# Performance work log

Hardware: AMD Instinct MI355X
Metric: run time of the kernel (lower is better)

## Reference

```python
import jax, jax.numpy as jnp
import numpy as np

NUM_HEADS = 4

def _proj(x, w, b):
    # Conv1d kernel_size=1 == pointwise linear over channels: [B, Cin, N] -> [B, Cout, N]
    return jnp.einsum('oi,bin->bon', w, x) + b[None, :, None]

def setup_inputs() -> dict:
    key = jax.random.key(0)
    ks = jax.random.split(key, 11)
    B, D, N = 8, 256, 2048
    inp = {
        'query': jax.random.normal(ks[0], (B, D, N), jnp.float32),
        'key':   jax.random.normal(ks[1], (B, D, N), jnp.float32),
        'value': jax.random.normal(ks[2], (B, D, N), jnp.float32),
        'w_q': jax.random.normal(ks[3], (D, D), jnp.float32) * (1.0 / np.sqrt(D)),
        'b_q': jax.random.normal(ks[4], (D,), jnp.float32) * 0.02,
        'w_k': jax.random.normal(ks[5], (D, D), jnp.float32) * (1.0 / np.sqrt(D)),
        'b_k': jax.random.normal(ks[6], (D,), jnp.float32) * 0.02,
        'w_v': jax.random.normal(ks[7], (D, D), jnp.float32) * (1.0 / np.sqrt(D)),
        'b_v': jax.random.normal(ks[8], (D,), jnp.float32) * 0.02,
        'w_m': jax.random.normal(ks[9], (D, D), jnp.float32) * (1.0 / np.sqrt(D)),
        'b_m': jax.random.normal(ks[10], (D,), jnp.float32) * 0.02,
    }
    return inp

def reference(query, key, value, w_q, b_q, w_k, b_k, w_v, b_v, w_m, b_m):
    B, D, N = query.shape
    H = NUM_HEADS
    d = D // H  # head dim (outer slot of channel split, matching torch .view)
    q = _proj(query, w_q, b_q).reshape(B, d, H, N)
    k = _proj(key,   w_k, b_k).reshape(B, d, H, N)
    v = _proj(value, w_v, b_v).reshape(B, d, H, N)
    scale = jnp.asarray(1.0 / np.sqrt(d), q.dtype)
    scores = jnp.einsum('bdhn,bdhm->bhnm', q, k) * scale  # [B,H,N,N]
    prob = jax.nn.softmax(scores, axis=-1)
    x = jnp.einsum('bhnm,bdhm->bdhn', prob, v)            # [B,d,H,N]
    out = _proj(x.reshape(B, D, N), w_m, b_m)             # [B,D,N]
    return out
```

## Files before the change

kernel.cpp:

```cpp
#include <hip/hip_runtime.h>
#include <cstdint>
#include <cstddef>

typedef unsigned short u16;
typedef unsigned int   u32;
typedef __attribute__((ext_vector_type(4))) float f32x4;
typedef __attribute__((ext_vector_type(16))) float f32x16;
typedef __attribute__((ext_vector_type(8))) short bf16x8;
typedef __attribute__((ext_vector_type(4))) unsigned short u16x4;
typedef __attribute__((ext_vector_type(2))) u32 u32x2;
typedef __attribute__((ext_vector_type(4))) u32 u32x4;

#define DEVI static __device__ __forceinline__
#define MFMA16(a,b,c) __builtin_amdgcn_mfma_f32_16x16x32_bf16((a),(b),(c),0,0,0)
#define MFMA32(a,b,c) __builtin_amdgcn_mfma_f32_32x32x16_bf16((a),(b),(c),0,0,0)

DEVI u16 f2b(float f) {
  u32 u = __builtin_bit_cast(u32, f);
  u32 r = u + 0x7fffu + ((u >> 16) & 1u);
  return (u16)(r >> 16);
}

DEVI u32 pkbf(float a, float b) {
  u32 r;
  asm("v_cvt_pk_bf16_f32 %0, %1, %2" : "=v"(r) : "v"(a), "v"(b));
  return r;
}

DEVI void load_lds16(const void* g, void* l) {
  __builtin_amdgcn_global_load_lds(
      (const __attribute__((address_space(1))) u32*)g,
      (__attribute__((address_space(3))) u32*)l, 16, 0, 0);
}

DEVI int perm_o(int o) { return 4 * (o & 63) + (o >> 6); }

__global__ __launch_bounds__(256) void k_prep_w(
    const float* __restrict__ wq, const float* __restrict__ wk,
    const float* __restrict__ wv, const float* __restrict__ wm,
    const float* __restrict__ bq, const float* __restrict__ bk, const float* __restrict__ bv,
    u16* __restrict__ WQ, u16* __restrict__ WK, u16* __restrict__ WV, u16* __restrict__ WM,
    float* __restrict__ BQ, float* __restrict__ BK, float* __restrict__ BV)
{
  int row = blockIdx.x, t = threadIdx.x, m = blockIdx.y;
  if (m == 0)      WQ[row * 256 + t] = f2b(wq[perm_o(row) * 256 + t]);
  else if (m == 1) WK[row * 256 + t] = f2b(wk[perm_o(row) * 256 + t]);
  else if (m == 2) WV[row * 256 + t] = f2b(wv[perm_o(row) * 256 + t]);
  else if (m == 3) WM[row * 256 + t] = f2b(wm[row * 256 + perm_o(t)]);
  else if (row == 0) {
    BQ[t] = bq[perm_o(t)];
    BK[t] = bk[perm_o(t)];
    BV[t] = bv[perm_o(t)];
  }
}

__global__ __launch_bounds__(256) void k_transpose(
    const float* __restrict__ q, const float* __restrict__ k, const float* __restrict__ v,
    u16* __restrict__ xq, u16* __restrict__ xk, u16* __restrict__ xv)
{
  __shared__ u16 tile[64][68];
  const int N = 2048, D = 256;
  int n0 = blockIdx.x * 64, c0 = blockIdx.y * 64;
  int b = blockIdx.z & 7, which = blockIdx.z >> 3;
  const float* src = (which == 0 ? q : which == 1 ? k : v) + (size_t)b * D * N;
  u16* dst = (which == 0 ? xq : which == 1 ? xk : xv) + (size_t)b * N * D;
  int t = threadIdx.x;
  int cl = t >> 4, ng = t & 15;
#pragma unroll
  for (int cc = 0; cc < 4; ++cc) {
    int c = cl + 16 * cc;
    f32x4 val = *(const f32x4*)&src[(size_t)(c0 + c) * N + n0 + ng * 4];
#pragma unroll
    for (int j = 0; j < 4; ++j) tile[c][ng * 4 + j] = f2b(val[j]);
  }
  __syncthreads();
  int n = t & 63, cq = t >> 6;
  union { u16 s[16]; u32x4 v4[2]; } pk;
#pragma unroll
  for (int j = 0; j < 16; ++j) pk.s[j] = tile[cq * 16 + j][n];
  u32x4* o = (u32x4*)&dst[(size_t)(n0 + n) * D + c0 + cq * 16];
  o[0] = pk.v4[0];
  o[1] = pk.v4[1];
}

template<int EPI>
__global__ __launch_bounds__(256, 4) void k_gemm(
    const u16* __restrict__ A, long sA,
    const u16* __restrict__ Bm, long sB,
    const float* __restrict__ bias,
    void* __restrict__ out, long sOut)
{
  __shared__ u16 lA[64 * 64];
  __shared__ u16 lB[64 * 64];
  int t = threadIdx.x, b = blockIdx.z;
  const u16* Ab = A + (size_t)b * sA + (size_t)blockIdx.x * 64 * 256;
  const u16* Bb = Bm + (size_t)b * sB + (size_t)blockIdx.y * 64 * 256;
  int l = t & 63, w = t >> 6, g = l >> 4, col = l & 15;
  int wr = w >> 1, wc = w & 1;
  f32x4 acc[2][2] = {};
  u32 sOf[2], sDs[2];
#pragma unroll
  for (int j = 0; j < 2; ++j) {
    int c = t + 256 * j;
    sOf[j] = (u32)(((c >> 3) * 512) + (((c & 7) ^ ((c >> 3) & 7)) << 4));
    sDs[j] = (u32)(c * 16);
  }
  for (int k0 = 0; k0 < 256; k0 += 64) {
    __syncthreads();
#pragma unroll
    for (int j = 0; j < 2; ++j) {
      load_lds16((const char*)(Ab + k0) + sOf[j], (char*)lA + sDs[j]);
      load_lds16((const char*)(Bb + k0) + sOf[j], (char*)lB + sDs[j]);
    }
    asm volatile("s_waitcnt vmcnt(0)" ::: "memory");
    __syncthreads();
#pragma unroll
    for (int kc = 0; kc < 2; ++kc) {
      bf16x8 af[2], bfr[2];
#pragma unroll
      for (int mt = 0; mt < 2; ++mt) {
        int row = wr * 32 + mt * 16 + col;
        af[mt] = *(const bf16x8*)((const char*)lA + row * 128 + (((kc * 4 + g) ^ (row & 7)) << 4));
      }
#pragma unroll
      for (int nt = 0; nt < 2; ++nt) {
        int row = wc * 32 + nt * 16 + col;
        bfr[nt] = *(const bf16x8*)((const char*)lB + row * 128 + (((kc * 4 + g) ^ (row & 7)) << 4));
      }
#pragma unroll
      for (int mt = 0; mt < 2; ++mt)
#pragma unroll
        for (int nt = 0; nt < 2; ++nt)
          acc[mt][nt] = MFMA16(af[mt], bfr[nt], acc[mt][nt]);
    }
  }
  if (EPI == 0) {
    u16* o = (u16*)out + (size_t)b * sOut;
#pragma unroll
    for (int nt = 0; nt < 2; ++nt) {
      int op = blockIdx.y * 64 + wc * 32 + nt * 16 + col;
      int hh = op >> 6, ii = op & 63;
      float bv = bias[op];
#pragma unroll
      for (int mt = 0; mt < 2; ++mt) {
        int nbase = blockIdx.x * 64 + wr * 32 + mt * 16 + g * 4;
#pragma unroll
        for (int r = 0; r < 4; ++r)
          o[((size_t)(hh * 2048 + nbase + r)) * 64 + ii] = f2b(acc[mt][nt][r] + bv);
      }
    }
  } else if (EPI == 1) {
    u16* o = (u16*)out + (size_t)b * sOut;
#pragma unroll
    for (int mt = 0; mt < 2; ++mt)
#pragma unroll
      for (int r = 0; r < 4; ++r) {
        int row = blockIdx.x * 64 + wr * 32 + mt * 16 + g * 4 + r;
        float bv = bias[row];
#pragma unroll
        for (int nt = 0; nt < 2; ++nt) {
          int cn = blockIdx.y * 64 + wc * 32 + nt * 16 + col;
          o[(size_t)row * 2048 + cn] = f2b(acc[mt][nt][r] + bv);
        }
      }
  } else {
    float* o = (float*)out + (size_t)b * sOut;
#pragma unroll
    for (int mt = 0; mt < 2; ++mt)
#pragma unroll
      for (int r = 0; r < 4; ++r) {
        int row = blockIdx.x * 64 + wr * 32 + mt * 16 + g * 4 + r;
        float bv = bias[row];
#pragma unroll
        for (int nt = 0; nt < 2; ++nt) {
          int cn = blockIdx.y * 64 + wc * 32 + nt * 16 + col;
          o[(size_t)row * 2048 + cn] = acc[mt][nt][r] + bv;
        }
      }
  }
}

__global__ __launch_bounds__(256, 4) void k_attn(
    const u16* __restrict__ Qt, const u16* __restrict__ Kt,
    const u16* __restrict__ Vw, u16* __restrict__ Xws)
{
  __shared__ union {
    u16 stg[2][2][4096];
    float cmb[2][64][36];
  } sh;
  const float SC2 = 0.18033688011112042f;
  int t = threadIdx.x, l = t & 63, w = t >> 6;
  int hi = l >> 5, col = l & 31;
  int qh = w & 1, kvh = w >> 1;
  int nb = blockIdx.x, hh = blockIdx.y, b = blockIdx.z;
  const u16* Qb = Qt + ((size_t)(b * 4 + hh) * 2048) * 64;
  const u16* Kb = Kt + ((size_t)(b * 4 + hh) * 2048) * 64;
  const u16* Vb = Vw + ((size_t)(b * 256 + hh * 64)) * 2048;
  int nq = nb * 64 + qh * 32 + col;

  bf16x8 qf[4];
#pragma unroll
  for (int ks = 0; ks < 4; ++ks)
    qf[ks] = *(const bf16x8*)&Qb[(size_t)nq * 64 + ks * 16 + hi * 8];

  int tp = t & 127;
  u32 kSrc[4], vSrc[4], sDst[4];
#pragma unroll
  for (int j = 0; j < 4; ++j) {
    int c = tp + 128 * j;
    int r = c >> 3, c16 = c & 7;
    kSrc[j] = (u32)((r * 128 + c16 * 16) ^ ((r & 7) << 4));
    vSrc[j] = (u32)(r * 4096 + ((c16 ^ (r & 7)) << 4));
    sDst[j] = (u32)(c * 16);
  }
  u32 offC[4];
#pragma unroll
  for (int ks = 0; ks < 4; ++ks)
    offC[ks] = (u32)(((2 * ks + hi) ^ (col & 7)) << 4);
  const char* kBase0 = (const char*)sh.stg[kvh][0] + col * 128;
  const char* vBase0 = (const char*)sh.stg[kvh][1] + col * 128;

  f32x16 xac[2] = {};
  float psum = 0.0f, m_run = 0.0f;

  for (int it = 0; it < 16; ++it) {
    __syncthreads();
    int tile = kvh * 16 + it;
    const char* kb = (const char*)Kb + (size_t)tile * 8192;
    const char* vb = (const char*)Vb + (size_t)tile * 128;
#pragma unroll
    for (int j = 0; j < 4; ++j)
      load_lds16(kb + kSrc[j], (char*)sh.stg[kvh][0] + sDst[j]);
#pragma unroll
    for (int j = 0; j < 4; ++j)
      load_lds16(vb + vSrc[j], (char*)sh.stg[kvh][1] + sDst[j]);

    if (__any(psum > 16777216.0f)) {
      const float ds = 5.9604644775390625e-8f;
      xac[0] *= ds; xac[1] *= ds;
      psum *= ds;
      m_run += 24.0f;
    }
    asm volatile("s_waitcnt vmcnt(0)" ::: "memory");
    __syncthreads();

    f32x16 sac[2] = {};
    __builtin_amdgcn_s_setprio(1);
#pragma unroll
    for (int ks = 0; ks < 4; ++ks) {
      bf16x8 kf0 = *(const bf16x8*)(kBase0 + offC[ks]);
      bf16x8 kf1 = *(const bf16x8*)(kBase0 + 4096 + offC[ks]);
      sac[0] = MFMA32(kf0, qf[ks], sac[0]);
      sac[1] = MFMA32(kf1, qf[ks], sac[1]);
    }
    __builtin_amdgcn_s_setprio(0);

    bf16x8 pf[4];
#pragma unroll
    for (int mt = 0; mt < 2; ++mt) {
      float p[16];
#pragma unroll
      for (int r = 0; r < 16; ++r) {
        p[r] = __builtin_amdgcn_exp2f(__builtin_fmaf(sac[mt][r], SC2, -m_run));
        psum += p[r];
      }
      u32 A0 = pkbf(p[0],  p[1]),  B0 = pkbf(p[2],  p[3]);
      u32 A1 = pkbf(p[4],  p[5]),  B1 = pkbf(p[6],  p[7]);
      u32 A2 = pkbf(p[8],  p[9]),  B2 = pkbf(p[10], p[11]);
      u32 A3 = pkbf(p[12], p[13]), B3 = pkbf(p[14], p[15]);
      asm("v_permlane32_swap_b32 %0, %1" : "+v"(A0), "+v"(A1));
      asm("v_permlane32_swap_b32 %0, %1" : "+v"(B0), "+v"(B1));
      asm("v_permlane32_swap_b32 %0, %1" : "+v"(A2), "+v"(A3));
      asm("v_permlane32_swap_b32 %0, %1" : "+v"(B2), "+v"(B3));
      union { u32 u[4]; bf16x8 v; } f0, f1;
      f0.u[0] = A0; f0.u[1] = B0; f0.u[2] = A1; f0.u[3] = B1;
      f1.u[0] = A2; f1.u[1] = B2; f1.u[2] = A3; f1.u[3] = B3;
      pf[mt * 2 + 0] = f0.v;
      pf[mt * 2 + 1] = f1.v;
    }

    __builtin_amdgcn_s_setprio(1);
#pragma unroll
    for (int S = 0; S < 4; ++S) {
      bf16x8 vf0 = *(const bf16x8*)(vBase0 + offC[S]);
      bf16x8 vf1 = *(const bf16x8*)(vBase0 + 4096 + offC[S]);
      xac[0] = MFMA32(vf0, pf[S], xac[0]);
      xac[1] = MFMA32(vf1, pf[S], xac[1]);
    }
    __builtin_amdgcn_s_setprio(0);
  }

  __syncthreads();
  if (kvh == 1) {
    float* d = &sh.cmb[qh][l][0];
#pragma unroll
    for (int r = 0; r < 16; ++r) { d[r] = xac[0][r]; d[16 + r] = xac[1][r]; }
    d[32] = psum; d[33] = m_run;
  }
  __syncthreads();
  if (kvh == 0) {
    const float* s = &sh.cmb[qh][l][0];
    float m1 = s[33], ps1 = s[32];
    float M = fmaxf(m_run, m1);
    float f0 = __builtin_amdgcn_exp2f(m_run - M);
    float f1 = __builtin_amdgcn_exp2f(m1 - M);
    float den = psum * f0 + ps1 * f1;
    den += __shfl_xor(den, 32);
    float inv = 1.0f / den;
    u16* Ob = Xws + (size_t)b * 2048 * 256 + (size_t)nq * 256 + hh * 64;
#pragma unroll
    for (int it2 = 0; it2 < 2; ++it2) {
#pragma unroll
      for (int rq = 0; rq < 4; ++rq) {
        float v0 = (xac[it2][4 * rq + 0] * f0 + s[it2 * 16 + 4 * rq + 0] * f1) * inv;
        float v1 = (xac[it2][4 * rq + 1] * f0 + s[it2 * 16 + 4 * rq + 1] * f1) * inv;
        float v2 = (xac[it2][4 * rq + 2] * f0 + s[it2 * 16 + 4 * rq + 2] * f1) * inv;
        float v3 = (xac[it2][4 * rq + 3] * f0 + s[it2 * 16 + 4 * rq + 3] * f1) * inv;
        u32x2 w2; w2[0] = pkbf(v0, v1); w2[1] = pkbf(v2, v3);
        *(u32x2*)&Ob[it2 * 32 + 8 * rq + 4 * hi] = w2;
      }
    }
  }
}

extern "C" void kernel_launch(void* const* d_in, const int* in_sizes, int n_in,
                              void* d_out, int out_size, void* d_ws, size_t ws_size,
                              hipStream_t stream)
{
  const float* q_in = (const float*)d_in[0];
  const float* k_in = (const float*)d_in[1];
  const float* v_in = (const float*)d_in[2];
  const float* w_q  = (const float*)d_in[3];
  const float* b_q  = (const float*)d_in[4];
  const float* w_k  = (const float*)d_in[5];
  const float* b_k  = (const float*)d_in[6];
  const float* w_v  = (const float*)d_in[7];
  const float* b_v  = (const float*)d_in[8];
  const float* w_m  = (const float*)d_in[9];
  const float* b_m  = (const float*)d_in[10];

  char* ws = (char*)d_ws;
  u16* XT_Q = (u16*)(ws + 0);
  u16* XT_K = (u16*)(ws + 8388608);
  u16* XT_V = (u16*)(ws + 16777216);
  u16* QT   = (u16*)(ws + 25165824);
  u16* KT   = (u16*)(ws + 33554432);
  u16* VW   = (u16*)(ws + 41943040);
  u16* WQ   = (u16*)(ws + 50331648);
  u16* WK   = (u16*)(ws + 50462720);
  u16* WV   = (u16*)(ws + 50593792);
  u16* WM   = (u16*)(ws + 50724864);
  float* BQ = (float*)(ws + 50855936);
  float* BK = (float*)(ws + 50856960);
  float* BV = (float*)(ws + 50857984);

  k_prep_w<<<dim3(256, 5), 256, 0, stream>>>(w_q, w_k, w_v, w_m, b_q, b_k, b_v,
                                             WQ, WK, WV, WM, BQ, BK, BV);
  k_transpose<<<dim3(32, 4, 24), 256, 0, stream>>>(q_in, k_in, v_in, XT_Q, XT_K, XT_V);
  k_gemm<0><<<dim3(32, 4, 8), 256, 0, stream>>>(XT_Q, 2048L * 256, WQ, 0, BQ, QT, 4L * 2048 * 64);
  k_gemm<0><<<dim3(32, 4, 8), 256, 0, stream>>>(XT_K, 2048L * 256, WK, 0, BK, KT, 4L * 2048 * 64);
  k_gemm<1><<<dim3(4, 32, 8), 256, 0, stream>>>(WV, 0, XT_V, 2048L * 256, BV, VW, 256L * 2048);
  k_attn<<<dim3(32, 4, 8), 256, 0, stream>>>(QT, KT, VW, XT_Q);
  k_gemm<2><<<dim3(4, 32, 8), 256, 0, stream>>>(WM, 0, XT_Q, 2048L * 256, b_m, d_out, 256L * 2048);
}
```

Before: 110.6 us.

## Double-buffer LDS staging in GEMM and attention; restructure attention work split

```diff
diff --git a/kernel.cpp b/kernel.cpp
--- a/kernel.cpp
+++ b/kernel.cpp
@@ -90,8 +90,8 @@
     const float* __restrict__ bias,
     void* __restrict__ out, long sOut)
 {
-  __shared__ u16 lA[64 * 64];
-  __shared__ u16 lB[64 * 64];
+  __shared__ u16 lA[2][64 * 64];
+  __shared__ u16 lB[2][64 * 64];
   int t = threadIdx.x, b = blockIdx.z;
   const u16* Ab = A + (size_t)b * sA + (size_t)blockIdx.x * 64 * 256;
   const u16* Bb = Bm + (size_t)b * sB + (size_t)blockIdx.y * 64 * 256;
@@ -101,18 +101,27 @@
   u32 sOf[2], sDs[2];
 #pragma unroll
   for (int j = 0; j < 2; ++j) {
-    int c = t + 256 * j;
-    sOf[j] = (u32)(((c >> 3) * 512) + (((c & 7) ^ ((c >> 3) & 7)) << 4));
-    sDs[j] = (u32)(c * 16);
-  }
-  for (int k0 = 0; k0 < 256; k0 += 64) {
-    __syncthreads();
+    int ci = t + 256 * j;
+    int r = ci >> 3, c = ci & 7;
+    sOf[j] = (u32)(r * 512 + ((c ^ (r & 7)) << 4));
+    sDs[j] = (u32)(ci * 16);
+  }
+  auto stage = [&](int buf, int k0) {
 #pragma unroll
     for (int j = 0; j < 2; ++j) {
-      load_lds16((const char*)(Ab + k0) + sOf[j], (char*)lA + sDs[j]);
-      load_lds16((const char*)(Bb + k0) + sOf[j], (char*)lB + sDs[j]);
-    }
-    asm volatile("s_waitcnt vmcnt(0)" ::: "memory");
+      load_lds16((const char*)Ab + k0 * 2 + sOf[j], (char*)lA[buf] + sDs[j]);
+      load_lds16((const char*)Bb + k0 * 2 + sOf[j], (char*)lB[buf] + sDs[j]);
+    }
+  };
+  stage(0, 0);
+  for (int s = 0; s < 4; ++s) {
+    int cur = s & 1;
+    if (s < 3) {
+      stage(cur ^ 1, (s + 1) * 64);
+      asm volatile("s_waitcnt vmcnt(4)" ::: "memory");
+    } else {
+      asm volatile("s_waitcnt vmcnt(0)" ::: "memory");
+    }
     __syncthreads();
 #pragma unroll
     for (int kc = 0; kc < 2; ++kc) {
@@ -120,12 +129,12 @@
 #pragma unroll
       for (int mt = 0; mt < 2; ++mt) {
         int row = wr * 32 + mt * 16 + col;
-        af[mt] = *(const bf16x8*)((const char*)lA + row * 128 + (((kc * 4 + g) ^ (row & 7)) << 4));
+        af[mt] = *(const bf16x8*)((const char*)lA[cur] + row * 128 + (((kc * 4 + g) ^ (row & 7)) << 4));
       }
 #pragma unroll
       for (int nt = 0; nt < 2; ++nt) {
         int row = wc * 32 + nt * 16 + col;
-        bfr[nt] = *(const bf16x8*)((const char*)lB + row * 128 + (((kc * 4 + g) ^ (row & 7)) << 4));
+        bfr[nt] = *(const bf16x8*)((const char*)lB[cur] + row * 128 + (((kc * 4 + g) ^ (row & 7)) << 4));
       }
 #pragma unroll
       for (int mt = 0; mt < 2; ++mt)
@@ -133,6 +142,7 @@
         for (int nt = 0; nt < 2; ++nt)
           acc[mt][nt] = MFMA16(af[mt], bfr[nt], acc[mt][nt]);
     }
+    __syncthreads();
   }
   if (EPI == 0) {
     u16* o = (u16*)out + (size_t)b * sOut;
@@ -180,88 +190,92 @@
   }
 }
 
-__global__ __launch_bounds__(256, 4) void k_attn(
+__global__ __launch_bounds__(256, 2) void k_attn(
     const u16* __restrict__ Qt, const u16* __restrict__ Kt,
     const u16* __restrict__ Vw, u16* __restrict__ Xws)
 {
-  __shared__ union {
-    u16 stg[2][2][4096];
-    float cmb[2][64][36];
-  } sh;
+  __shared__ u16 stg[2][2][4096];
   const float SC2 = 0.18033688011112042f;
   int t = threadIdx.x, l = t & 63, w = t >> 6;
   int hi = l >> 5, col = l & 31;
-  int qh = w & 1, kvh = w >> 1;
   int nb = blockIdx.x, hh = blockIdx.y, b = blockIdx.z;
   const u16* Qb = Qt + ((size_t)(b * 4 + hh) * 2048) * 64;
   const u16* Kb = Kt + ((size_t)(b * 4 + hh) * 2048) * 64;
   const u16* Vb = Vw + ((size_t)(b * 256 + hh * 64)) * 2048;
-  int nq = nb * 64 + qh * 32 + col;
+  int nq = nb * 128 + w * 32 + col;
 
   bf16x8 qf[4];
 #pragma unroll
   for (int ks = 0; ks < 4; ++ks)
     qf[ks] = *(const bf16x8*)&Qb[(size_t)nq * 64 + ks * 16 + hi * 8];
 
-  int tp = t & 127;
-  u32 kSrc[4], vSrc[4], sDst[4];
-#pragma unroll
-  for (int j = 0; j < 4; ++j) {
-    int c = tp + 128 * j;
-    int r = c >> 3, c16 = c & 7;
-    kSrc[j] = (u32)((r * 128 + c16 * 16) ^ ((r & 7) << 4));
-    vSrc[j] = (u32)(r * 4096 + ((c16 ^ (r & 7)) << 4));
-    sDst[j] = (u32)(c * 16);
+  u32 kSrc[2], vSrc[2], sDst[2];
+#pragma unroll
+  for (int j = 0; j < 2; ++j) {
+    int ci = t + 256 * j;
+    int r = ci >> 3, c = ci & 7;
+    u32 sw = (u32)((c ^ ((r >> 2) & 7)) << 4);
+    kSrc[j] = (u32)(r * 128) + sw;
+    vSrc[j] = (u32)(r * 4096) + sw;
+    sDst[j] = (u32)(ci * 16);
   }
   u32 offC[4];
 #pragma unroll
   for (int ks = 0; ks < 4; ++ks)
-    offC[ks] = (u32)(((2 * ks + hi) ^ (col & 7)) << 4);
-  const char* kBase0 = (const char*)sh.stg[kvh][0] + col * 128;
-  const char* vBase0 = (const char*)sh.stg[kvh][1] + col * 128;
-
-  f32x16 xac[2] = {};
+    offC[ks] = (u32)(((2 * ks + hi) ^ ((col >> 2) & 7)) << 4);
+
+  f32x16 xac0 = {}, xac1 = {};
   float psum = 0.0f, m_run = 0.0f;
 
-  for (int it = 0; it < 16; ++it) {
-    __syncthreads();
-    int tile = kvh * 16 + it;
+  auto stage = [&](int buf, int tile) {
     const char* kb = (const char*)Kb + (size_t)tile * 8192;
     const char* vb = (const char*)Vb + (size_t)tile * 128;
 #pragma unroll
-    for (int j = 0; j < 4; ++j)
-      load_lds16(kb + kSrc[j], (char*)sh.stg[kvh][0] + sDst[j]);
-#pragma unroll
-    for (int j = 0; j < 4; ++j)
-      load_lds16(vb + vSrc[j], (char*)sh.stg[kvh][1] + sDst[j]);
-
-    if (__any(psum > 16777216.0f)) {
-      const float ds = 5.9604644775390625e-8f;
-      xac[0] *= ds; xac[1] *= ds;
-      psum *= ds;
-      m_run += 24.0f;
-    }
-    asm volatile("s_waitcnt vmcnt(0)" ::: "memory");
+    for (int j = 0; j < 2; ++j)
+      load_lds16(kb + kSrc[j], (char*)stg[buf][0] + sDst[j]);
+#pragma unroll
+    for (int j = 0; j < 2; ++j)
+      load_lds16(vb + vSrc[j], (char*)stg[buf][1] + sDst[j]);
+  };
+
+  stage(0, 0);
+  for (int it = 0; it < 32; ++it) {
+    int cur = it & 1;
+    if (it < 31) {
+      stage(cur ^ 1, it + 1);
+      if (__any(psum > 16777216.0f)) {
+        const float ds = 5.9604644775390625e-8f;
+        xac0 *= ds; xac1 *= ds;
+        psum *= ds;
+        m_run += 24.0f;
+      }
+      asm volatile("s_waitcnt vmcnt(4)" ::: "memory");
+    } else {
+      asm volatile("s_waitcnt vmcnt(0)" ::: "memory");
+    }
     __syncthreads();
-
-    f32x16 sac[2] = {};
+    const char* kK = (const char*)stg[cur][0] + col * 128;
+    const char* kV = (const char*)stg[cur][1] + col * 128;
+
+    f32x16 sac0 = {}, sac1 = {};
     __builtin_amdgcn_s_setprio(1);
 #pragma unroll
     for (int ks = 0; ks < 4; ++ks) {
-      bf16x8 kf0 = *(const bf16x8*)(kBase0 + offC[ks]);
-      bf16x8 kf1 = *(const bf16x8*)(kBase0 + 4096 + offC[ks]);
-      sac[0] = MFMA32(kf0, qf[ks], sac[0]);
-      sac[1] = MFMA32(kf1, qf[ks], sac[1]);
+      bf16x8 kf0 = *(const bf16x8*)(kK + offC[ks]);
+      bf16x8 kf1 = *(const bf16x8*)(kK + 4096 + offC[ks]);
+      sac0 = MFMA32(kf0, qf[ks], sac0);
+      sac1 = MFMA32(kf1, qf[ks], sac1);
     }
     __builtin_amdgcn_s_setprio(0);
 
     bf16x8 pf[4];
 #pragma unroll
     for (int mt = 0; mt < 2; ++mt) {
+      const f32x16& sc = mt ? sac1 : sac0;
       float p[16];
 #pragma unroll
       for (int r = 0; r < 16; ++r) {
-        p[r] = __builtin_amdgcn_exp2f(__builtin_fmaf(sac[mt][r], SC2, -m_run));
+        p[r] = __builtin_amdgcn_exp2f(__builtin_fmaf(sc[r], SC2, -m_run));
         psum += p[r];
       }
       u32 A0 = pkbf(p[0],  p[1]),  B0 = pkbf(p[2],  p[3]);
@@ -282,43 +296,29 @@
     __builtin_amdgcn_s_setprio(1);
 #pragma unroll
     for (int S = 0; S < 4; ++S) {
-      bf16x8 vf0 = *(const bf16x8*)(vBase0 + offC[S]);
-      bf16x8 vf1 = *(const bf16x8*)(vBase0 + 4096 + offC[S]);
-      xac[0] = MFMA32(vf0, pf[S], xac[0]);
-      xac[1] = MFMA32(vf1, pf[S], xac[1]);
+      bf16x8 vf0 = *(const bf16x8*)(kV + offC[S]);
+      bf16x8 vf1 = *(const bf16x8*)(kV + 4096 + offC[S]);
+      xac0 = MFMA32(vf0, pf[S], xac0);
+      xac1 = MFMA32(vf1, pf[S], xac1);
     }
     __builtin_amdgcn_s_setprio(0);
-  }
-
-  __syncthreads();
-  if (kvh == 1) {
-    float* d = &sh.cmb[qh][l][0];
-#pragma unroll
-    for (int r = 0; r < 16; ++r) { d[r] = xac[0][r]; d[16 + r] = xac[1][r]; }
-    d[32] = psum; d[33] = m_run;
-  }
-  __syncthreads();
-  if (kvh == 0) {
-    const float* s = &sh.cmb[qh][l][0];
-    float m1 = s[33], ps1 = s[32];
-    float M = fmaxf(m_run, m1);
-    float f0 = __builtin_amdgcn_exp2f(m_run - M);
-    float f1 = __builtin_amdgcn_exp2f(m1 - M);
-    float den = psum * f0 + ps1 * f1;
-    den += __shfl_xor(den, 32);
-    float inv = 1.0f / den;
-    u16* Ob = Xws + (size_t)b * 2048 * 256 + (size_t)nq * 256 + hh * 64;
-#pragma unroll
-    for (int it2 = 0; it2 < 2; ++it2) {
-#pragma unroll
-      for (int rq = 0; rq < 4; ++rq) {
-        float v0 = (xac[it2][4 * rq + 0] * f0 + s[it2 * 16 + 4 * rq + 0] * f1) * inv;
-        float v1 = (xac[it2][4 * rq + 1] * f0 + s[it2 * 16 + 4 * rq + 1] * f1) * inv;
-        float v2 = (xac[it2][4 * rq + 2] * f0 + s[it2 * 16 + 4 * rq + 2] * f1) * inv;
-        float v3 = (xac[it2][4 * rq + 3] * f0 + s[it2 * 16 + 4 * rq + 3] * f1) * inv;
-        u32x2 w2; w2[0] = pkbf(v0, v1); w2[1] = pkbf(v2, v3);
-        *(u32x2*)&Ob[it2 * 32 + 8 * rq + 4 * hi] = w2;
-      }
+    __syncthreads();
+  }
+
+  psum += __shfl_xor(psum, 32);
+  float inv = 1.0f / psum;
+  u16* Ob = Xws + (size_t)b * 2048 * 256 + (size_t)nq * 256 + hh * 64;
+#pragma unroll
+  for (int it2 = 0; it2 < 2; ++it2) {
+    const f32x16& xa = it2 ? xac1 : xac0;
+#pragma unroll
+    for (int rq = 0; rq < 4; ++rq) {
+      float v0 = xa[4 * rq + 0] * inv;
+      float v1 = xa[4 * rq + 1] * inv;
+      float v2 = xa[4 * rq + 2] * inv;
+      float v3 = xa[4 * rq + 3] * inv;
+      u32x2 w2; w2[0] = pkbf(v0, v1); w2[1] = pkbf(v2, v3);
+      *(u32x2*)&Ob[it2 * 32 + 8 * rq + 4 * hi] = w2;
     }
   }
 }
@@ -360,6 +360,6 @@
   k_gemm<0><<<dim3(32, 4, 8), 256, 0, stream>>>(XT_Q, 2048L * 256, WQ, 0, BQ, QT, 4L * 2048 * 64);
   k_gemm<0><<<dim3(32, 4, 8), 256, 0, stream>>>(XT_K, 2048L * 256, WK, 0, BK, KT, 4L * 2048 * 64);
   k_gemm<1><<<dim3(4, 32, 8), 256, 0, stream>>>(WV, 0, XT_V, 2048L * 256, BV, VW, 256L * 2048);
-  k_attn<<<dim3(32, 4, 8), 256, 0, stream>>>(QT, KT, VW, XT_Q);
+  k_attn<<<dim3(16, 4, 8), 256, 0, stream>>>(QT, KT, VW, XT_Q);
   k_gemm<2><<<dim3(4, 32, 8), 256, 0, stream>>>(WM, 0, XT_Q, 2048L * 256, b_m, d_out, 256L * 2048);
 }
```

Result: no change. 108.6 us (-1.9%).
